# Performance work log

Measured on AMD Instinct MI355X. Metric: run time of the kernel, lower is better.

## Reference

```python
import jax, jax.numpy as jnp
import numpy as np

N_EMBED = 1024
HEAD_SIZE = 128
B, T = 4, 2048

def setup_inputs() -> dict:
    key = jax.random.key(0)
    kx, kq, kk, kv = jax.random.split(key, 4)
    bound = 1.0 / np.sqrt(N_EMBED)  # torch Linear default init range
    x = jax.random.normal(kx, (B, T, N_EMBED), dtype=jnp.float32)
    Wq = jax.random.uniform(kq, (N_EMBED, HEAD_SIZE), jnp.float32, -bound, bound)
    Wk = jax.random.uniform(kk, (N_EMBED, HEAD_SIZE), jnp.float32, -bound, bound)
    Wv = jax.random.uniform(kv, (N_EMBED, HEAD_SIZE), jnp.float32, -bound, bound)
    return {"x": x, "Wq": Wq, "Wk": Wk, "Wv": Wv}

def reference(x, Wq, Wk, Wv):
    Bn, Tn, C = x.shape
    q = x @ Wq  # [B,T,H]
    k = x @ Wk
    v = x @ Wv
    # NOTE: original scales by C**-0.5 where C = n_embed (not head_size)
    scale = C ** (-0.5)
    wei = jnp.einsum('bqh,bkh->bqk', q, k) * scale  # [B,T,T]
    causal = jnp.tril(jnp.ones((Tn, Tn), dtype=bool))
    wei = jnp.where(causal, wei, -jnp.inf)
    wei = jax.nn.softmax(wei, axis=-1)
    # dropout p=0.0 -> identity
    return jnp.einsum('bqk,bkh->bqh', wei, v)
```

## Files before the change

kernel.cpp:

```cpp
#include <hip/hip_runtime.h>
#include <stdint.h>

#define B_ 4
#define T_ 2048
#define C_ 1024
#define H_ 128
#define NEG_BIG -3.0e38f

typedef __attribute__((ext_vector_type(8))) short short8;
typedef __attribute__((ext_vector_type(4))) float f32x4;
typedef __attribute__((ext_vector_type(4))) unsigned short ushort4v;
typedef __attribute__((ext_vector_type(8))) unsigned short ushort8v;

__device__ __forceinline__ unsigned short f2bf(float f) {
  union { float f; unsigned u; } cv; cv.f = f;
  return (unsigned short)((cv.u + 0x8000u) >> 16);
}

__device__ __forceinline__ float bf2f(unsigned short s) {
  union { unsigned u; float f; } cv; cv.u = ((unsigned)s) << 16;
  return cv.f;
}

__device__ __forceinline__ void gld16(const void* g, void* l) {
  __builtin_amdgcn_global_load_lds(
      (const __attribute__((address_space(1))) unsigned int*)g,
      (__attribute__((address_space(3))) unsigned int*)l, 16, 0, 0);
}

#define CSCALE 0.045084220027780106f

__global__ __launch_bounds__(256) void prep_w(const float* __restrict__ Wq,
                                              const float* __restrict__ Wk,
                                              const float* __restrict__ Wv,
                                              unsigned short* __restrict__ WbT) {
  const int i = blockIdx.x * 256 + threadIdx.x;
  const int linear = i * 4;
  const int j = linear >> 10;
  const int k0 = linear & 1023;
  const float* W = (j < 128) ? Wq : (j < 256) ? Wk : Wv;
  const int h = j & 127;
  ushort4v p;
  p[0] = f2bf(W[(k0 + 0) * 128 + h]);
  p[1] = f2bf(W[(k0 + 1) * 128 + h]);
  p[2] = f2bf(W[(k0 + 2) * 128 + h]);
  p[3] = f2bf(W[(k0 + 3) * 128 + h]);
  *(ushort4v*)(WbT + linear) = p;
}

__global__ __launch_bounds__(256) void qkv_proj(const float* __restrict__ x,
                                                const unsigned short* __restrict__ WbT,
                                                unsigned short* __restrict__ Qb,
                                                unsigned short* __restrict__ Kb,
                                                unsigned short* __restrict__ VT) {
  __shared__ unsigned short As[2][128 * 64];
  __shared__ unsigned short Bs[2][96 * 64];

  const int tid  = threadIdx.x;
  const int wave = tid >> 6, lane = tid & 63;
  const int quad = lane >> 4, l15 = lane & 15;
  const int rb = blockIdx.x >> 2, cb = blockIdx.x & 3;
  const int gm0 = rb * 128, gn0 = cb * 96;
  const int wm = wave >> 1, wn = wave & 1;

  const int srow = lane >> 3, sslot = lane & 7;
  const int axr = tid >> 3, axc = tid & 7;
  const float* gAx = x + (size_t)(gm0 + axr) * C_ + axc * 8;

  int aoff[4][2], boff[3][2];
#pragma unroll
  for (int mt = 0; mt < 4; ++mt) {
    const int r = wm * 64 + mt * 16 + l15;
#pragma unroll
    for (int ks = 0; ks < 2; ++ks)
      aoff[mt][ks] = r * 64 + (((ks * 4 + quad) ^ r) & 7) * 8;
  }
#pragma unroll
  for (int nt = 0; nt < 3; ++nt) {
    const int r = wn * 48 + nt * 16 + l15;
#pragma unroll
    for (int ks = 0; ks < 2; ++ks)
      boff[nt][ks] = r * 64 + (((ks * 4 + quad) ^ r) & 7) * 8;
  }

  f32x4 acc[4][3];
  const f32x4 zero4 = {0.f, 0.f, 0.f, 0.f};
#pragma unroll
  for (int mt = 0; mt < 4; ++mt)
#pragma unroll
    for (int nt = 0; nt < 3; ++nt) acc[mt][nt] = zero4;

#define STAGE_B(buf, kb_)                                                          \
  {                                                                                \
    const int ko = (kb_) * 64;                                                     \
    _Pragma("unroll")                                                              \
    for (int q = 0; q < 3; ++q) {                                                  \
      const int row = wave * 24 + q * 8 + srow;                                    \
      gld16(WbT + (size_t)(gn0 + row) * C_ + ko + ((sslot ^ row) & 7) * 8,         \
            &Bs[buf][(wave * 24 + q * 8) * 64]);                                   \
    }                                                                              \
  }

#define LOAD_A(ko_)                                                                \
  _Pragma("unroll")                                                                \
  for (int q = 0; q < 4; ++q) {                                                    \
    av0[q] = *(const f32x4*)(gAx + (size_t)(q * 32) * C_ + (ko_));                 \
    av1[q] = *(const f32x4*)(gAx + (size_t)(q * 32) * C_ + (ko_) + 4);             \
  }

#define WRITE_A(buf)                                                               \
  _Pragma("unroll")                                                                \
  for (int q = 0; q < 4; ++q) {                                                    \
    const int row = axr + q * 32;                                                  \
    short8 aw;                                                                     \
    _Pragma("unroll")                                                              \
    for (int e = 0; e < 4; ++e) {                                                  \
      aw[e]     = (short)f2bf(av0[q][e]);                                          \
      aw[4 + e] = (short)f2bf(av1[q][e]);                                          \
    }                                                                              \
    *(short8*)(&As[buf][row * 64 + ((axc ^ row) & 7) * 8]) = aw;                   \
  }

  f32x4 av0[4], av1[4];
  LOAD_A(0);
  STAGE_B(0, 0);
  WRITE_A(0);

  for (int kb = 0; kb < 16; ++kb) {
    __syncthreads();
    const int cur = kb & 1, nxt = cur ^ 1;
    if (kb + 1 < 16) {
      LOAD_A((kb + 1) * 64);
      STAGE_B(nxt, kb + 1);
    }
    const unsigned short* Ac = As[cur];
    const unsigned short* Bc = Bs[cur];
#pragma unroll
    for (int ks = 0; ks < 2; ++ks) {
      short8 b0 = *(const short8*)(Bc + boff[0][ks]);
      short8 b1 = *(const short8*)(Bc + boff[1][ks]);
      short8 b2 = *(const short8*)(Bc + boff[2][ks]);
#pragma unroll
      for (int mt = 0; mt < 4; ++mt) {
        short8 a = *(const short8*)(Ac + aoff[mt][ks]);
        acc[mt][0] = __builtin_amdgcn_mfma_f32_16x16x32_bf16(a, b0, acc[mt][0], 0, 0, 0);
        acc[mt][1] = __builtin_amdgcn_mfma_f32_16x16x32_bf16(a, b1, acc[mt][1], 0, 0, 0);
        acc[mt][2] = __builtin_amdgcn_mfma_f32_16x16x32_bf16(a, b2, acc[mt][2], 0, 0, 0);
      }
    }
    if (kb + 1 < 16) WRITE_A(nxt);
  }
#undef STAGE_B
#undef LOAD_A
#undef WRITE_A

#pragma unroll
  for (int mt = 0; mt < 4; ++mt) {
    const int row0 = gm0 + wm * 64 + mt * 16 + quad * 4;
#pragma unroll
    for (int nt = 0; nt < 3; ++nt) {
      const int colbase = gn0 + wn * 48 + nt * 16;
      const int col = colbase + l15;
      if (colbase < 128) {
#pragma unroll
        for (int r = 0; r < 4; ++r)
          Qb[(size_t)(row0 + r) * H_ + col] = f2bf(acc[mt][nt][r] * CSCALE);
      } else if (colbase < 256) {
#pragma unroll
        for (int r = 0; r < 4; ++r)
          Kb[(size_t)(row0 + r) * H_ + (col - 128)] = f2bf(acc[mt][nt][r]);
      } else {
        const int h = col - 256;
        const int bidx = row0 >> 11;
        const int t0 = row0 & 2047;
        ushort4v pk;
        pk[0] = f2bf(acc[mt][nt][0]); pk[1] = f2bf(acc[mt][nt][1]);
        pk[2] = f2bf(acc[mt][nt][2]); pk[3] = f2bf(acc[mt][nt][3]);
        *(ushort4v*)(VT + (size_t)(bidx * H_ + h) * T_ + t0) = pk;
      }
    }
  }
}

__global__ __launch_bounds__(256, 2) void attn1(const unsigned short* __restrict__ Qb,
                                                const unsigned short* __restrict__ Kb,
                                                const unsigned short* __restrict__ VT,
                                                unsigned short* __restrict__ Opart,
                                                float* __restrict__ mpart,
                                                float* __restrict__ lpart,
                                                float* __restrict__ out) {
  __shared__ unsigned short Ks[2][64 * 128];
  __shared__ unsigned short Vs[2][128 * 64];
  __shared__ unsigned short Pls[4][16 * 72];
  __shared__ float Als[4][16];

  const int bid = blockIdx.x;
  const int b  = bid & 3;
  const int j  = (bid >> 2) & 31;
  const int ch = bid >> 7;
  if (ch * 8 > j) return;
  const int ntiles = min(8, j + 1 - ch * 8);

  const int tid  = threadIdx.x;
  const int wave = tid >> 6, lane = tid & 63;
  const int quad = lane >> 4, l15 = lane & 15;

  const unsigned short* qrow = Qb + (size_t)(b * T_ + j * 64 + wave * 16 + l15) * H_;
  short8 aq[4];
#pragma unroll
  for (int ks = 0; ks < 4; ++ks)
    aq[ks] = *(const short8*)(qrow + ks * 32 + quad * 8);

  const unsigned short* Kb_b = Kb + (size_t)(b * T_) * H_;
  const unsigned short* VT_b = VT + (size_t)(b * H_) * T_;

  const int k_row4 = lane >> 4, k_slot = lane & 15;
  const int v_row8 = lane >> 3, v_slot = lane & 7;

#define STAGE_KV(buf, kv0_)                                                        \
  {                                                                                \
    _Pragma("unroll")                                                              \
    for (int i = 0; i < 4; ++i) {                                                  \
      const int r = wave * 16 + i * 4 + k_row4;                                    \
      const int c2 = (k_slot & 8) | ((k_slot ^ r) & 7);                            \
      gld16(Kb_b + (size_t)((kv0_) + r) * H_ + c2 * 8,                             \
            &Ks[buf][(wave * 16 + i * 4) * 128]);                                  \
    }                                                                              \
    _Pragma("unroll")                                                              \
    for (int i = 0; i < 4; ++i) {                                                  \
      const int h = wave * 32 + i * 8 + v_row8;                                    \
      gld16(VT_b + (size_t)h * T_ + (kv0_) + ((v_slot ^ h) & 7) * 8,               \
            &Vs[buf][(wave * 32 + i * 8) * 64]);                                   \
    }                                                                              \
  }

  STAGE_KV(0, ch * 512);

  const f32x4 zero4 = {0.f, 0.f, 0.f, 0.f};
  f32x4 O[8];
#pragma unroll
  for (int nth = 0; nth < 8; ++nth) O[nth] = zero4;
  float m_ = NEG_BIG, l_ = 0.f;

  for (int t = 0; t < ntiles; ++t) {
    __syncthreads();
    const int kv0 = ch * 512 + t * 64;
    if (t + 1 < ntiles) STAGE_KV((t + 1) & 1, kv0 + 64);

    const unsigned short* kb = Ks[t & 1];
    f32x4 ST[4];
    ST[0] = zero4; ST[1] = zero4; ST[2] = zero4; ST[3] = zero4;
#pragma unroll
    for (int ntl = 0; ntl < 4; ++ntl) {
      const int kvr = ntl * 16 + l15;
#pragma unroll
      for (int ks = 0; ks < 4; ++ks) {
        const int c = ks * 4 + quad;
        const int slot = (c & 8) | ((c ^ kvr) & 7);
        short8 kf = *(const short8*)(kb + kvr * 128 + slot * 8);
        ST[ntl] = __builtin_amdgcn_mfma_f32_16x16x32_bf16(kf, aq[ks], ST[ntl], 0, 0, 0);
      }
    }

    if (ch * 8 + t == j) {
      const int ql = j * 64 + wave * 16 + l15;
#pragma unroll
      for (int ntl = 0; ntl < 4; ++ntl)
#pragma unroll
        for (int r = 0; r < 4; ++r) {
          const int kl = kv0 + ntl * 16 + quad * 4 + r;
          if (kl > ql) ST[ntl][r] = NEG_BIG;
        }
    }

    float vmax = ST[0][0];
#pragma unroll
    for (int ntl = 0; ntl < 4; ++ntl)
#pragma unroll
      for (int r = 0; r < 4; ++r) vmax = fmaxf(vmax, ST[ntl][r]);
    vmax = fmaxf(vmax, __shfl_xor(vmax, 16));
    vmax = fmaxf(vmax, __shfl_xor(vmax, 32));
    const float mn = fmaxf(m_, vmax);
    const float alpha = __builtin_amdgcn_exp2f(m_ - mn);
    m_ = mn;
    float s = 0.f;
#pragma unroll
    for (int ntl = 0; ntl < 4; ++ntl)
#pragma unroll
      for (int r = 0; r < 4; ++r) {
        const float p = __builtin_amdgcn_exp2f(ST[ntl][r] - mn);
        ST[ntl][r] = p;
        s += p;
      }
    s += __shfl_xor(s, 16);
    s += __shfl_xor(s, 32);
    l_ = l_ * alpha + s;

#pragma unroll
    for (int ntl = 0; ntl < 4; ++ntl) {
      ushort4v pk;
      pk[0] = f2bf(ST[ntl][0]); pk[1] = f2bf(ST[ntl][1]);
      pk[2] = f2bf(ST[ntl][2]); pk[3] = f2bf(ST[ntl][3]);
      *(ushort4v*)(&Pls[wave][l15 * 72 + ntl * 16 + quad * 4]) = pk;
    }

    if (lane < 16) Als[wave][lane] = alpha;
    if (!__all(alpha == 1.f)) {
      f32x4 al4 = *(const f32x4*)&Als[wave][quad * 4];
#pragma unroll
      for (int nth = 0; nth < 8; ++nth)
#pragma unroll
        for (int r = 0; r < 4; ++r) O[nth][r] *= al4[r];
    }

    const unsigned short* vb = Vs[t & 1];
    short8 ap0 = *(const short8*)(&Pls[wave][l15 * 72 + quad * 8]);
    short8 ap1 = *(const short8*)(&Pls[wave][l15 * 72 + 32 + quad * 8]);
#pragma unroll
    for (int nth = 0; nth < 8; ++nth) {
      const int h = nth * 16 + l15;
      short8 v0 = *(const short8*)(vb + h * 64 + ((quad ^ h) & 7) * 8);
      short8 v1 = *(const short8*)(vb + h * 64 + (((4 + quad) ^ h) & 7) * 8);
      O[nth] = __builtin_amdgcn_mfma_f32_16x16x32_bf16(ap0, v0, O[nth], 0, 0, 0);
      O[nth] = __builtin_amdgcn_mfma_f32_16x16x32_bf16(ap1, v1, O[nth], 0, 0, 0);
    }
  }
#undef STAGE_KV

  if ((j >> 3) == 0) {
    if (lane < 16) Als[wave][lane] = 1.0f / l_;
    f32x4 li4 = *(const f32x4*)&Als[wave][quad * 4];
    float* op = out + (size_t)(b * T_ + j * 64 + wave * 16) * H_;
#pragma unroll
    for (int nth = 0; nth < 8; ++nth)
#pragma unroll
      for (int r = 0; r < 4; ++r)
        op[(quad * 4 + r) * H_ + nth * 16 + l15] = O[nth][r] * li4[r];
  } else {
    const int pid = (b * 32 + j) * 4 + ch;
    unsigned short* po = Opart + (size_t)(pid * 64 + wave * 16) * H_;
#pragma unroll
    for (int nth = 0; nth < 8; ++nth)
#pragma unroll
      for (int r = 0; r < 4; ++r)
        po[(quad * 4 + r) * H_ + nth * 16 + l15] = f2bf(O[nth][r]);
    if (lane < 16) {
      mpart[pid * 64 + wave * 16 + lane] = m_;
      lpart[pid * 64 + wave * 16 + lane] = l_;
    }
  }
}

__global__ __launch_bounds__(256) void attn2(const unsigned short* __restrict__ Opart,
                                             const float* __restrict__ mpart,
                                             const float* __restrict__ lpart,
                                             float* __restrict__ out) {
  const int b = blockIdx.x & 3;
  const int j = 8 + (blockIdx.x >> 2);
  const int nch = (j >> 3) + 1;
  const int tid = threadIdx.x;
  const int qh = tid >> 4;
  const int h0 = (tid & 15) * 8;
  const int pbase = (b * 32 + j) * 4;

#pragma unroll
  for (int i = 0; i < 4; ++i) {
    const int q = qh + i * 16;
    float m_fin = NEG_BIG;
    for (int ch = 0; ch < nch; ++ch)
      m_fin = fmaxf(m_fin, mpart[(pbase + ch) * 64 + q]);
    float lf = 0.f;
    float o[8];
#pragma unroll
    for (int c = 0; c < 8; ++c) o[c] = 0.f;
    for (int ch = 0; ch < nch; ++ch) {
      const int pid = pbase + ch;
      const float sc = __builtin_amdgcn_exp2f(mpart[pid * 64 + q] - m_fin);
      lf += sc * lpart[pid * 64 + q];
      ushort8v pv = *(const ushort8v*)(Opart + (size_t)(pid * 64 + q) * H_ + h0);
#pragma unroll
      for (int c = 0; c < 8; ++c) o[c] += sc * bf2f(pv[c]);
    }
    const float inv = 1.0f / lf;
    float* op = out + (size_t)(b * T_ + j * 64 + q) * H_ + h0;
    f32x4 v0 = {o[0] * inv, o[1] * inv, o[2] * inv, o[3] * inv};
    f32x4 v1 = {o[4] * inv, o[5] * inv, o[6] * inv, o[7] * inv};
    *(f32x4*)(op) = v0;
    *(f32x4*)(op + 4) = v1;
  }
}

extern "C" void kernel_launch(void* const* d_in, const int* in_sizes, int n_in,
                              void* d_out, int out_size, void* d_ws, size_t ws_size,
                              hipStream_t stream) {
  const float* x  = (const float*)d_in[0];
  const float* Wq = (const float*)d_in[1];
  const float* Wk = (const float*)d_in[2];
  const float* Wv = (const float*)d_in[3];
  float* out = (float*)d_out;

  char* ws = (char*)d_ws;
  unsigned short* WbT = (unsigned short*)(ws);
  unsigned short* Qb  = (unsigned short*)(ws + 1048576);
  unsigned short* Kb  = (unsigned short*)(ws + 3145728);
  unsigned short* VT  = (unsigned short*)(ws + 5242880);
  unsigned short* Opart = (unsigned short*)(ws + 8388608);
  float* mpart = (float*)(ws + 16777216);
  float* lpart = (float*)(ws + 16908288);

  prep_w<<<dim3(384), dim3(256), 0, stream>>>(Wq, Wk, Wv, WbT);
  qkv_proj<<<dim3(256), dim3(256), 0, stream>>>(x, WbT, Qb, Kb, VT);
  attn1<<<dim3(512), dim3(256), 0, stream>>>(Qb, Kb, VT, Opart, mpart, lpart, out);
  attn2<<<dim3(96), dim3(256), 0, stream>>>(Opart, mpart, lpart, out);
}
```

Before: 137.8 us.

## Balance causal attention work by pairing query tiles and striding KV chunks

The attention kernel now pairs query tile j with tile 31-j in each block and splits each query tile's KV range across 8 chunks by stride, so every block gets a roughly equal number of KV tiles instead of the triangular imbalance. All query tiles now write partial results and are merged in the combine kernel, which now covers every tile. The projection GEMM switches to 64-row tiles with 512 blocks and two blocks per CU for better occupancy. The cost is more partial-output traffic and a larger reduction pass.

```diff
diff --git a/kernel.cpp b/kernel.cpp
--- a/kernel.cpp
+++ b/kernel.cpp
@@ -48,29 +48,29 @@
   *(ushort4v*)(WbT + linear) = p;
 }
 
-__global__ __launch_bounds__(256) void qkv_proj(const float* __restrict__ x,
-                                                const unsigned short* __restrict__ WbT,
-                                                unsigned short* __restrict__ Qb,
-                                                unsigned short* __restrict__ Kb,
-                                                unsigned short* __restrict__ VT) {
-  __shared__ unsigned short As[2][128 * 64];
+__global__ __launch_bounds__(256, 2) void qkv_proj(const float* __restrict__ x,
+                                                   const unsigned short* __restrict__ WbT,
+                                                   unsigned short* __restrict__ Qb,
+                                                   unsigned short* __restrict__ Kb,
+                                                   unsigned short* __restrict__ VT) {
+  __shared__ unsigned short As[2][64 * 64];
   __shared__ unsigned short Bs[2][96 * 64];
 
   const int tid  = threadIdx.x;
   const int wave = tid >> 6, lane = tid & 63;
   const int quad = lane >> 4, l15 = lane & 15;
-  const int rb = blockIdx.x >> 2, cb = blockIdx.x & 3;
-  const int gm0 = rb * 128, gn0 = cb * 96;
+  const int rb = blockIdx.x & 127, cb = blockIdx.x >> 7;
+  const int gm0 = rb * 64, gn0 = cb * 96;
   const int wm = wave >> 1, wn = wave & 1;
 
   const int srow = lane >> 3, sslot = lane & 7;
   const int axr = tid >> 3, axc = tid & 7;
   const float* gAx = x + (size_t)(gm0 + axr) * C_ + axc * 8;
 
-  int aoff[4][2], boff[3][2];
-#pragma unroll
-  for (int mt = 0; mt < 4; ++mt) {
-    const int r = wm * 64 + mt * 16 + l15;
+  int aoff[2][2], boff[3][2];
+#pragma unroll
+  for (int mt = 0; mt < 2; ++mt) {
+    const int r = wm * 32 + mt * 16 + l15;
 #pragma unroll
     for (int ks = 0; ks < 2; ++ks)
       aoff[mt][ks] = r * 64 + (((ks * 4 + quad) ^ r) & 7) * 8;
@@ -83,10 +83,10 @@
       boff[nt][ks] = r * 64 + (((ks * 4 + quad) ^ r) & 7) * 8;
   }
 
-  f32x4 acc[4][3];
+  f32x4 acc[2][3];
   const f32x4 zero4 = {0.f, 0.f, 0.f, 0.f};
 #pragma unroll
-  for (int mt = 0; mt < 4; ++mt)
+  for (int mt = 0; mt < 2; ++mt)
 #pragma unroll
     for (int nt = 0; nt < 3; ++nt) acc[mt][nt] = zero4;
 
@@ -103,14 +103,14 @@
 
 #define LOAD_A(ko_)                                                                \
   _Pragma("unroll")                                                                \
-  for (int q = 0; q < 4; ++q) {                                                    \
+  for (int q = 0; q < 2; ++q) {                                                    \
     av0[q] = *(const f32x4*)(gAx + (size_t)(q * 32) * C_ + (ko_));                 \
     av1[q] = *(const f32x4*)(gAx + (size_t)(q * 32) * C_ + (ko_) + 4);             \
   }
 
 #define WRITE_A(buf)                                                               \
   _Pragma("unroll")                                                                \
-  for (int q = 0; q < 4; ++q) {                                                    \
+  for (int q = 0; q < 2; ++q) {                                                    \
     const int row = axr + q * 32;                                                  \
     short8 aw;                                                                     \
     _Pragma("unroll")                                                              \
@@ -121,7 +121,7 @@
     *(short8*)(&As[buf][row * 64 + ((axc ^ row) & 7) * 8]) = aw;                   \
   }
 
-  f32x4 av0[4], av1[4];
+  f32x4 av0[2], av1[2];
   LOAD_A(0);
   STAGE_B(0, 0);
   WRITE_A(0);
@@ -141,7 +141,7 @@
       short8 b1 = *(const short8*)(Bc + boff[1][ks]);
       short8 b2 = *(const short8*)(Bc + boff[2][ks]);
 #pragma unroll
-      for (int mt = 0; mt < 4; ++mt) {
+      for (int mt = 0; mt < 2; ++mt) {
         short8 a = *(const short8*)(Ac + aoff[mt][ks]);
         acc[mt][0] = __builtin_amdgcn_mfma_f32_16x16x32_bf16(a, b0, acc[mt][0], 0, 0, 0);
         acc[mt][1] = __builtin_amdgcn_mfma_f32_16x16x32_bf16(a, b1, acc[mt][1], 0, 0, 0);
@@ -155,8 +155,8 @@
 #undef WRITE_A
 
 #pragma unroll
-  for (int mt = 0; mt < 4; ++mt) {
-    const int row0 = gm0 + wm * 64 + mt * 16 + quad * 4;
+  for (int mt = 0; mt < 2; ++mt) {
+    const int row0 = gm0 + wm * 32 + mt * 16 + quad * 4;
 #pragma unroll
     for (int nt = 0; nt < 3; ++nt) {
       const int colbase = gn0 + wn * 48 + nt * 16;
@@ -187,8 +187,7 @@
                                                 const unsigned short* __restrict__ VT,
                                                 unsigned short* __restrict__ Opart,
                                                 float* __restrict__ mpart,
-                                                float* __restrict__ lpart,
-                                                float* __restrict__ out) {
+                                                float* __restrict__ lpart) {
   __shared__ unsigned short Ks[2][64 * 128];
   __shared__ unsigned short Vs[2][128 * 64];
   __shared__ unsigned short Pls[4][16 * 72];
@@ -196,21 +195,17 @@
 
   const int bid = blockIdx.x;
   const int b  = bid & 3;
-  const int j  = (bid >> 2) & 31;
-  const int ch = bid >> 7;
-  if (ch * 8 > j) return;
-  const int ntiles = min(8, j + 1 - ch * 8);
+  const int jp = (bid >> 2) & 15;
+  const int ch = bid >> 6;
+  const int j1 = jp, j2 = 31 - jp;
+  const int n1 = (ch <= j1) ? (((j1 - ch) >> 3) + 1) : 0;
+  const int n2 = ((j2 - ch) >> 3) + 1;
+  const int ntt = n1 + n2;
 
   const int tid  = threadIdx.x;
   const int wave = tid >> 6, lane = tid & 63;
   const int quad = lane >> 4, l15 = lane & 15;
 
-  const unsigned short* qrow = Qb + (size_t)(b * T_ + j * 64 + wave * 16 + l15) * H_;
-  short8 aq[4];
-#pragma unroll
-  for (int ks = 0; ks < 4; ++ks)
-    aq[ks] = *(const short8*)(qrow + ks * 32 + quad * 8);
-
   const unsigned short* Kb_b = Kb + (size_t)(b * T_) * H_;
   const unsigned short* VT_b = VT + (size_t)(b * H_) * T_;
 
@@ -220,21 +215,45 @@
 #define STAGE_KV(buf, kv0_)                                                        \
   {                                                                                \
     _Pragma("unroll")                                                              \
-    for (int i = 0; i < 4; ++i) {                                                  \
-      const int r = wave * 16 + i * 4 + k_row4;                                    \
+    for (int i_ = 0; i_ < 4; ++i_) {                                               \
+      const int r = wave * 16 + i_ * 4 + k_row4;                                   \
       const int c2 = (k_slot & 8) | ((k_slot ^ r) & 7);                            \
       gld16(Kb_b + (size_t)((kv0_) + r) * H_ + c2 * 8,                             \
-            &Ks[buf][(wave * 16 + i * 4) * 128]);                                  \
+            &Ks[buf][(wave * 16 + i_ * 4) * 128]);                                 \
     }                                                                              \
     _Pragma("unroll")                                                              \
-    for (int i = 0; i < 4; ++i) {                                                  \
-      const int h = wave * 32 + i * 8 + v_row8;                                    \
+    for (int i_ = 0; i_ < 4; ++i_) {                                               \
+      const int h = wave * 32 + i_ * 8 + v_row8;                                   \
       gld16(VT_b + (size_t)h * T_ + (kv0_) + ((v_slot ^ h) & 7) * 8,               \
-            &Vs[buf][(wave * 32 + i * 8) * 64]);                                   \
+            &Vs[buf][(wave * 32 + i_ * 8) * 64]);                                  \
     }                                                                              \
   }
 
-  STAGE_KV(0, ch * 512);
+#define EPI(jr_)                                                                   \
+  {                                                                                \
+    const int pid = (b * 32 + (jr_)) * 8 + ch;                                     \
+    unsigned short* po = Opart + (size_t)(pid * 64 + wave * 16) * H_;              \
+    _Pragma("unroll")                                                              \
+    for (int nth = 0; nth < 8; ++nth)                                              \
+      _Pragma("unroll")                                                            \
+      for (int r = 0; r < 4; ++r)                                                  \
+        po[(quad * 4 + r) * H_ + nth * 16 + l15] = f2bf(O[nth][r]);                \
+    if (lane < 16) {                                                               \
+      mpart[pid * 64 + wave * 16 + lane] = m_;                                     \
+      lpart[pid * 64 + wave * 16 + lane] = l_;                                     \
+    }                                                                              \
+  }
+
+  int jr_cur = n1 ? j1 : j2;
+  short8 aq[4];
+  {
+    const unsigned short* qrow = Qb + (size_t)(b * T_ + jr_cur * 64 + wave * 16 + l15) * H_;
+#pragma unroll
+    for (int ks = 0; ks < 4; ++ks)
+      aq[ks] = *(const short8*)(qrow + ks * 32 + quad * 8);
+  }
+
+  STAGE_KV(0, ch * 64);
 
   const f32x4 zero4 = {0.f, 0.f, 0.f, 0.f};
   f32x4 O[8];
@@ -242,12 +261,28 @@
   for (int nth = 0; nth < 8; ++nth) O[nth] = zero4;
   float m_ = NEG_BIG, l_ = 0.f;
 
-  for (int t = 0; t < ntiles; ++t) {
+  for (int i = 0; i < ntt; ++i) {
     __syncthreads();
-    const int kv0 = ch * 512 + t * 64;
-    if (t + 1 < ntiles) STAGE_KV((t + 1) & 1, kv0 + 64);
-
-    const unsigned short* kb = Ks[t & 1];
+    if (i + 1 < ntt) {
+      const int in_ = i + 1;
+      const int tn = (in_ < n1) ? (ch + (in_ << 3)) : (ch + ((in_ - n1) << 3));
+      STAGE_KV((in_) & 1, tn * 64);
+    }
+    if (n1 && i == n1) {
+      EPI(j1);
+      m_ = NEG_BIG; l_ = 0.f;
+#pragma unroll
+      for (int nth = 0; nth < 8; ++nth) O[nth] = zero4;
+      jr_cur = j2;
+      const unsigned short* qrow = Qb + (size_t)(b * T_ + j2 * 64 + wave * 16 + l15) * H_;
+#pragma unroll
+      for (int ks = 0; ks < 4; ++ks)
+        aq[ks] = *(const short8*)(qrow + ks * 32 + quad * 8);
+    }
+    const int ti  = (i < n1) ? (ch + (i << 3)) : (ch + ((i - n1) << 3));
+    const int kv0 = ti * 64;
+
+    const unsigned short* kb = Ks[i & 1];
     f32x4 ST[4];
     ST[0] = zero4; ST[1] = zero4; ST[2] = zero4; ST[3] = zero4;
 #pragma unroll
@@ -262,8 +297,8 @@
       }
     }
 
-    if (ch * 8 + t == j) {
-      const int ql = j * 64 + wave * 16 + l15;
+    if (ti == jr_cur) {
+      const int ql = jr_cur * 64 + wave * 16 + l15;
 #pragma unroll
       for (int ntl = 0; ntl < 4; ++ntl)
 #pragma unroll
@@ -313,7 +348,7 @@
         for (int r = 0; r < 4; ++r) O[nth][r] *= al4[r];
     }
 
-    const unsigned short* vb = Vs[t & 1];
+    const unsigned short* vb = Vs[i & 1];
     short8 ap0 = *(const short8*)(&Pls[wave][l15 * 72 + quad * 8]);
     short8 ap1 = *(const short8*)(&Pls[wave][l15 * 72 + 32 + quad * 8]);
 #pragma unroll
@@ -325,30 +360,9 @@
       O[nth] = __builtin_amdgcn_mfma_f32_16x16x32_bf16(ap1, v1, O[nth], 0, 0, 0);
     }
   }
+  EPI(j2);
 #undef STAGE_KV
-
-  if ((j >> 3) == 0) {
-    if (lane < 16) Als[wave][lane] = 1.0f / l_;
-    f32x4 li4 = *(const f32x4*)&Als[wave][quad * 4];
-    float* op = out + (size_t)(b * T_ + j * 64 + wave * 16) * H_;
-#pragma unroll
-    for (int nth = 0; nth < 8; ++nth)
-#pragma unroll
-      for (int r = 0; r < 4; ++r)
-        op[(quad * 4 + r) * H_ + nth * 16 + l15] = O[nth][r] * li4[r];
-  } else {
-    const int pid = (b * 32 + j) * 4 + ch;
-    unsigned short* po = Opart + (size_t)(pid * 64 + wave * 16) * H_;
-#pragma unroll
-    for (int nth = 0; nth < 8; ++nth)
-#pragma unroll
-      for (int r = 0; r < 4; ++r)
-        po[(quad * 4 + r) * H_ + nth * 16 + l15] = f2bf(O[nth][r]);
-    if (lane < 16) {
-      mpart[pid * 64 + wave * 16 + lane] = m_;
-      lpart[pid * 64 + wave * 16 + lane] = l_;
-    }
-  }
+#undef EPI
 }
 
 __global__ __launch_bounds__(256) void attn2(const unsigned short* __restrict__ Opart,
@@ -356,12 +370,12 @@
                                              const float* __restrict__ lpart,
                                              float* __restrict__ out) {
   const int b = blockIdx.x & 3;
-  const int j = 8 + (blockIdx.x >> 2);
-  const int nch = (j >> 3) + 1;
+  const int j = blockIdx.x >> 2;
+  const int nch = min(j + 1, 8);
   const int tid = threadIdx.x;
   const int qh = tid >> 4;
   const int h0 = (tid & 15) * 8;
-  const int pbase = (b * 32 + j) * 4;
+  const int pbase = (b * 32 + j) * 8;
 
 #pragma unroll
   for (int i = 0; i < 4; ++i) {
@@ -405,11 +419,11 @@
   unsigned short* Kb  = (unsigned short*)(ws + 3145728);
   unsigned short* VT  = (unsigned short*)(ws + 5242880);
   unsigned short* Opart = (unsigned short*)(ws + 8388608);
-  float* mpart = (float*)(ws + 16777216);
-  float* lpart = (float*)(ws + 16908288);
+  float* mpart = (float*)(ws + 25165824);
+  float* lpart = (float*)(ws + 25427968);
 
   prep_w<<<dim3(384), dim3(256), 0, stream>>>(Wq, Wk, Wv, WbT);
-  qkv_proj<<<dim3(256), dim3(256), 0, stream>>>(x, WbT, Qb, Kb, VT);
-  attn1<<<dim3(512), dim3(256), 0, stream>>>(Qb, Kb, VT, Opart, mpart, lpart, out);
-  attn2<<<dim3(96), dim3(256), 0, stream>>>(Opart, mpart, lpart, out);
-}
+  qkv_proj<<<dim3(512), dim3(256), 0, stream>>>(x, WbT, Qb, Kb, VT);
+  attn1<<<dim3(512), dim3(256), 0, stream>>>(Qb, Kb, VT, Opart, mpart, lpart);
+  attn2<<<dim3(128), dim3(256), 0, stream>>>(Opart, mpart, lpart, out);
+}
```

Result: faster. 133.2 us (-3.3%).
